# Optimization experiments

Hardware: AMD Instinct MI355X
Metric: run time of the kernel (lower is better)

The kernel has to match this reference:

```python
import jax, jax.numpy as jnp
import numpy as np

B, IN, OUT = 1024, 512, 512

def setup_inputs() -> dict:
    key = jax.random.key(0)
    k1, k2 = jax.random.split(key)
    X = jax.random.normal(k1, (B, IN), dtype=jnp.float32)
    # init_std=0.02 path in the torch module: normal(std=0.02)
    W = jax.random.normal(k2, (OUT, IN), dtype=jnp.float32) * 0.02
    return {"X": X, "W": W}

def reference(X, W):
    # Tropical (min-plus) matmul: out[b, j] = min_i (X[b, i] + W[j, i])
    # Broadcast-add produces [B, OUT, IN]; min-reduce over IN.
    return jnp.min(X[:, None, :] + W[None, :, :], axis=-1)
```

## Files before the change

### kernel.cpp

```cpp
#include <hip/hip_runtime.h>
#include <math.h>


#define B_DIM   1024
#define IN_DIM  512
#define OUT_DIM 512

typedef unsigned int uint;

__device__ __forceinline__ uint pk2(float a, float b) {
    unsigned short ua = __builtin_bit_cast(unsigned short, (_Float16)a);
    unsigned short ub = __builtin_bit_cast(unsigned short, (_Float16)b);
    return (uint)ua | ((uint)ub << 16);
}

__device__ __forceinline__ float h_lo(uint u) {
    return (float)__builtin_bit_cast(_Float16, (unsigned short)(u & 0xffff));
}
__device__ __forceinline__ float h_hi(uint u) {
    return (float)__builtin_bit_cast(_Float16, (unsigned short)(u >> 16));
}

__device__ __forceinline__ uint pk_add_h(uint a, uint b) {
    uint d;
    asm("v_pk_add_f16 %0, %1, %2" : "=v"(d) : "v"(a), "v"(b));
    return d;
}
__device__ __forceinline__ uint pk_min_h(uint a, uint b) {
    uint d;
    asm("v_pk_min_f16 %0, %1, %2" : "=v"(d) : "v"(a), "v"(b));
    return d;
}

__global__ __launch_bounds__(256)
void MinPlus_pack_h(const float* __restrict__ X, const float* __restrict__ W,
                    uint* __restrict__ Xh, uint4* __restrict__ WT8) {
    const int tid = threadIdx.x;
    const int bid = blockIdx.x;

    if (bid < 64) {
        __shared__ float Ls[64][68];
        const int j0 = (bid & 7) * 64;
        const int k0 = (bid >> 3) * 64;
#pragma unroll
        for (int r = 0; r < 4; ++r) {
            const int jj = (tid >> 4) + r * 16;
            const int kq = tid & 15;
            const float4 v = *reinterpret_cast<const float4*>(&W[(j0 + jj) * IN_DIM + k0 + 4 * kq]);
            *reinterpret_cast<float4*>(&Ls[jj][4 * kq]) = v;
        }
        __syncthreads();
#pragma unroll
        for (int r = 0; r < 2; ++r) {
            const int idx = tid + r * 256;
            const int k8l = idx >> 6;
            const int jl  = idx & 63;
            const float4 a = *reinterpret_cast<const float4*>(&Ls[jl][8 * k8l]);
            const float4 b = *reinterpret_cast<const float4*>(&Ls[jl][8 * k8l + 4]);
            uint4 o;
            o.x = pk2(a.x, a.y); o.y = pk2(a.z, a.w);
            o.z = pk2(b.x, b.y); o.w = pk2(b.z, b.w);
            WT8[(size_t)(k0 / 8 + k8l) * OUT_DIM + j0 + jl] = o;
        }
    } else {
        const int cb = bid - 64;
        const float4* __restrict__ src = reinterpret_cast<const float4*>(X) + (size_t)cb * 512 + tid;
        uint2* __restrict__ dst = reinterpret_cast<uint2*>(Xh) + (size_t)cb * 512 + tid;
#pragma unroll
        for (int r = 0; r < 2; ++r) {
            const float4 v = src[r * 256];
            uint2 o;
            o.x = pk2(v.x, v.y);
            o.y = pk2(v.z, v.w);
            dst[r * 256] = o;
        }
    }
}

__global__ __launch_bounds__(1024)
void MinPlus_70832600646269_kernel(const uint* __restrict__ Xh,
                                   const uint4* __restrict__ WT8,
                                   float* __restrict__ out)
{
    __shared__ uint   Xs[8][256];
    __shared__ float4 part[16][8][64];

    const int tid  = threadIdx.x;
    const int lane = tid & 63;
    const int wid  = tid >> 6;
    const int j0   = blockIdx.x * 256;
    const int b0   = blockIdx.y * 8;

    if (tid < 512)
        reinterpret_cast<uint4*>(&Xs[0][0])[tid] =
            reinterpret_cast<const uint4*>(Xh + (size_t)b0 * 256)[tid];

    uint acc2[8][4];
#pragma unroll
    for (int b = 0; b < 8; ++b)
#pragma unroll
        for (int jq = 0; jq < 4; ++jq) acc2[b][jq] = 0x7C007C00u;

    const uint4* __restrict__ wbase = WT8 + j0 + lane;
    const int g0 = wid * 4;

    uint4 wA[4], wB[4];
#pragma unroll
    for (int jq = 0; jq < 4; ++jq)
        wA[jq] = wbase[(size_t)g0 * OUT_DIM + jq * 64];

    __syncthreads();

#define COMPUTE(WBUF, QT)                                                       \
    {                                                                           \
        _Pragma("unroll")                                                       \
        for (int b = 0; b < 8; ++b) {                                           \
            const uint4 x = *reinterpret_cast<const uint4*>(                    \
                &Xs[b][wid * 16 + (QT) * 4]);                                   \
            _Pragma("unroll")                                                   \
            for (int jq = 0; jq < 4; ++jq) {                                    \
                acc2[b][jq] = pk_min_h(acc2[b][jq], pk_add_h(WBUF[jq].x, x.x)); \
                acc2[b][jq] = pk_min_h(acc2[b][jq], pk_add_h(WBUF[jq].y, x.y)); \
                acc2[b][jq] = pk_min_h(acc2[b][jq], pk_add_h(WBUF[jq].z, x.z)); \
                acc2[b][jq] = pk_min_h(acc2[b][jq], pk_add_h(WBUF[jq].w, x.w)); \
            }                                                                   \
        }                                                                       \
    }

#pragma unroll
    for (int qt = 0; qt < 4; qt += 2) {
#pragma unroll
        for (int jq = 0; jq < 4; ++jq)
            wB[jq] = wbase[(size_t)(g0 + qt + 1) * OUT_DIM + jq * 64];

        COMPUTE(wA, qt)

        if (qt < 2) {
#pragma unroll
            for (int jq = 0; jq < 4; ++jq)
                wA[jq] = wbase[(size_t)(g0 + qt + 2) * OUT_DIM + jq * 64];
        }

        COMPUTE(wB, qt + 1)
    }
#undef COMPUTE

#pragma unroll
    for (int b = 0; b < 8; ++b) {
        float4 o;
        o.x = fminf(h_lo(acc2[b][0]), h_hi(acc2[b][0]));
        o.y = fminf(h_lo(acc2[b][1]), h_hi(acc2[b][1]));
        o.z = fminf(h_lo(acc2[b][2]), h_hi(acc2[b][2]));
        o.w = fminf(h_lo(acc2[b][3]), h_hi(acc2[b][3]));
        part[wid][b][lane] = o;
    }

    __syncthreads();

    if (tid < 512) {
        const int b = tid >> 6;
        const int l = tid & 63;
        float4 m = part[0][b][l];
#pragma unroll
        for (int p = 1; p < 16; ++p) {
            const float4 v = part[p][b][l];
            m.x = fminf(m.x, v.x);
            m.y = fminf(m.y, v.y);
            m.z = fminf(m.z, v.z);
            m.w = fminf(m.w, v.w);
        }
        float* orow = out + (size_t)(b0 + b) * OUT_DIM + j0;
        orow[l]       = m.x;
        orow[64 + l]  = m.y;
        orow[128 + l] = m.z;
        orow[192 + l] = m.w;
    }
}

extern "C" void kernel_launch(void* const* d_in, const int* in_sizes, int n_in,
                              void* d_out, int out_size, void* d_ws, size_t ws_size,
                              hipStream_t stream) {
    const float* X = (const float*)d_in[0];
    const float* W = (const float*)d_in[1];
    float* out = (float*)d_out;

    uint4* WT8 = (uint4*)d_ws;
    uint*  Xh  = (uint*)((char*)d_ws + (512 << 10));

    MinPlus_pack_h<<<dim3(64 + 256), 256, 0, stream>>>(X, W, Xh, WT8);

    MinPlus_70832600646269_kernel<<<dim3(OUT_DIM / 256, B_DIM / 8), 1024, 0, stream>>>(Xh, WT8, out);
}
```

Baseline: 21.94 us.

## Halve batch rows per block, drop W double-buffering, reduce partials in packed half

Each block now covers 4 batch rows instead of 8, so the grid doubles to 256 row-blocks and shared memory per block is halved. Launch bounds now request two blocks per CU. The W double-buffer prefetch is replaced by a simple non-unrolled loop that loads four W vectors per step, which lowers register pressure. The cross-wave reduction now keeps packed half pairs and uses pk_min, with all 1024 threads each writing one output. The cost is that every W element is loaded twice as often (less reuse per load) and the overlap of W loads with compute is lost, in exchange for higher occupancy and more parallelism.

```diff
diff --git a/kernel.cpp b/kernel.cpp
--- a/kernel.cpp
+++ b/kernel.cpp
@@ -77,103 +77,86 @@
     }
 }
 
-__global__ __launch_bounds__(1024)
+__global__ __launch_bounds__(1024, 2)
 void MinPlus_70832600646269_kernel(const uint* __restrict__ Xh,
                                    const uint4* __restrict__ WT8,
                                    float* __restrict__ out)
 {
-    __shared__ uint   Xs[8][256];
-    __shared__ float4 part[16][8][64];
+    __shared__ uint  Xs[4][256];
+    __shared__ uint4 part[16][4][64];
 
     const int tid  = threadIdx.x;
     const int lane = tid & 63;
     const int wid  = tid >> 6;
     const int j0   = blockIdx.x * 256;
-    const int b0   = blockIdx.y * 8;
+    const int b0   = blockIdx.y * 4;
 
-    if (tid < 512)
+    if (tid < 256)
         reinterpret_cast<uint4*>(&Xs[0][0])[tid] =
             reinterpret_cast<const uint4*>(Xh + (size_t)b0 * 256)[tid];
 
-    uint acc2[8][4];
+    uint acc2[4][4];
 #pragma unroll
-    for (int b = 0; b < 8; ++b)
+    for (int b = 0; b < 4; ++b)
 #pragma unroll
         for (int jq = 0; jq < 4; ++jq) acc2[b][jq] = 0x7C007C00u;
 
     const uint4* __restrict__ wbase = WT8 + j0 + lane;
     const int g0 = wid * 4;
 
-    uint4 wA[4], wB[4];
+    __syncthreads();
+
+#pragma unroll 1
+    for (int qt = 0; qt < 4; ++qt) {
+        uint4 w0 = wbase[(size_t)(g0 + qt) * OUT_DIM];
+        uint4 w1 = wbase[(size_t)(g0 + qt) * OUT_DIM + 64];
+        uint4 w2 = wbase[(size_t)(g0 + qt) * OUT_DIM + 128];
+        uint4 w3 = wbase[(size_t)(g0 + qt) * OUT_DIM + 192];
+
 #pragma unroll
-    for (int jq = 0; jq < 4; ++jq)
-        wA[jq] = wbase[(size_t)g0 * OUT_DIM + jq * 64];
+        for (int b = 0; b < 4; ++b) {
+            const uint4 x = *reinterpret_cast<const uint4*>(&Xs[b][wid * 16 + qt * 4]);
+
+            acc2[b][0] = pk_min_h(acc2[b][0], pk_add_h(w0.x, x.x));
+            acc2[b][0] = pk_min_h(acc2[b][0], pk_add_h(w0.y, x.y));
+            acc2[b][0] = pk_min_h(acc2[b][0], pk_add_h(w0.z, x.z));
+            acc2[b][0] = pk_min_h(acc2[b][0], pk_add_h(w0.w, x.w));
+
+            acc2[b][1] = pk_min_h(acc2[b][1], pk_add_h(w1.x, x.x));
+            acc2[b][1] = pk_min_h(acc2[b][1], pk_add_h(w1.y, x.y));
+            acc2[b][1] = pk_min_h(acc2[b][1], pk_add_h(w1.z, x.z));
+            acc2[b][1] = pk_min_h(acc2[b][1], pk_add_h(w1.w, x.w));
+
+            acc2[b][2] = pk_min_h(acc2[b][2], pk_add_h(w2.x, x.x));
+            acc2[b][2] = pk_min_h(acc2[b][2], pk_add_h(w2.y, x.y));
+            acc2[b][2] = pk_min_h(acc2[b][2], pk_add_h(w2.z, x.z));
+            acc2[b][2] = pk_min_h(acc2[b][2], pk_add_h(w2.w, x.w));
+
+            acc2[b][3] = pk_min_h(acc2[b][3], pk_add_h(w3.x, x.x));
+            acc2[b][3] = pk_min_h(acc2[b][3], pk_add_h(w3.y, x.y));
+            acc2[b][3] = pk_min_h(acc2[b][3], pk_add_h(w3.z, x.z));
+            acc2[b][3] = pk_min_h(acc2[b][3], pk_add_h(w3.w, x.w));
+        }
+    }
+
+#pragma unroll
+    for (int b = 0; b < 4; ++b)
+        part[wid][b][lane] = make_uint4(acc2[b][0], acc2[b][1], acc2[b][2], acc2[b][3]);
 
     __syncthreads();
 
-#define COMPUTE(WBUF, QT)                                                       \
-    {                                                                           \
-        _Pragma("unroll")                                                       \
-        for (int b = 0; b < 8; ++b) {                                           \
-            const uint4 x = *reinterpret_cast<const uint4*>(                    \
-                &Xs[b][wid * 16 + (QT) * 4]);                                   \
-            _Pragma("unroll")                                                   \
-            for (int jq = 0; jq < 4; ++jq) {                                    \
-                acc2[b][jq] = pk_min_h(acc2[b][jq], pk_add_h(WBUF[jq].x, x.x)); \
-                acc2[b][jq] = pk_min_h(acc2[b][jq], pk_add_h(WBUF[jq].y, x.y)); \
-                acc2[b][jq] = pk_min_h(acc2[b][jq], pk_add_h(WBUF[jq].z, x.z)); \
-                acc2[b][jq] = pk_min_h(acc2[b][jq], pk_add_h(WBUF[jq].w, x.w)); \
-            }                                                                   \
-        }                                                                       \
-    }
+    {
+        const int b  = tid >> 8;
+        const int jj = tid & 255;
+        const int l  = jj & 63;
+        const int c  = jj >> 6;
 
+        uint m = reinterpret_cast<const uint*>(&part[0][b][l])[c];
 #pragma unroll
-    for (int qt = 0; qt < 4; qt += 2) {
-#pragma unroll
-        for (int jq = 0; jq < 4; ++jq)
-            wB[jq] = wbase[(size_t)(g0 + qt + 1) * OUT_DIM + jq * 64];
+        for (int p = 1; p < 16; ++p)
+            m = pk_min_h(m, reinterpret_cast<const uint*>(&part[p][b][l])[c]);
 
-        COMPUTE(wA, qt)
-
-        if (qt < 2) {
-#pragma unroll
-            for (int jq = 0; jq < 4; ++jq)
-                wA[jq] = wbase[(size_t)(g0 + qt + 2) * OUT_DIM + jq * 64];
-        }
-
-        COMPUTE(wB, qt + 1)
-    }
-#undef COMPUTE
-
-#pragma unroll
-    for (int b = 0; b < 8; ++b) {
-        float4 o;
-        o.x = fminf(h_lo(acc2[b][0]), h_hi(acc2[b][0]));
-        o.y = fminf(h_lo(acc2[b][1]), h_hi(acc2[b][1]));
-        o.z = fminf(h_lo(acc2[b][2]), h_hi(acc2[b][2]));
-        o.w = fminf(h_lo(acc2[b][3]), h_hi(acc2[b][3]));
-        part[wid][b][lane] = o;
-    }
-
-    __syncthreads();
-
-    if (tid < 512) {
-        const int b = tid >> 6;
-        const int l = tid & 63;
-        float4 m = part[0][b][l];
-#pragma unroll
-        for (int p = 1; p < 16; ++p) {
-            const float4 v = part[p][b][l];
-            m.x = fminf(m.x, v.x);
-            m.y = fminf(m.y, v.y);
-            m.z = fminf(m.z, v.z);
-            m.w = fminf(m.w, v.w);
-        }
-        float* orow = out + (size_t)(b0 + b) * OUT_DIM + j0;
-        orow[l]       = m.x;
-        orow[64 + l]  = m.y;
-        orow[128 + l] = m.z;
-        orow[192 + l] = m.w;
+        out[(size_t)(b0 + b) * OUT_DIM + j0 + jj] = fminf(h_lo(m), h_hi(m));
     }
 }
 
@@ -189,5 +172,5 @@
 
     MinPlus_pack_h<<<dim3(64 + 256), 256, 0, stream>>>(X, W, Xh, WT8);
 
-    MinPlus_70832600646269_kernel<<<dim3(OUT_DIM / 256, B_DIM / 8), 1024, 0, stream>>>(Xh, WT8, out);
+    MinPlus_70832600646269_kernel<<<dim3(OUT_DIM / 256, B_DIM / 4), 1024, 0, stream>>>(Xh, WT8, out);
 }
```

New measurement: 23.42 us. 1.07x slower.
